# Performance work log

Measured on AMD Instinct MI355X. Metric: run time of the kernel, lower is better.

The kernel has to match this reference:

```python
import jax, jax.numpy as jnp
import numpy as np

DIM = 384
NH = 6
HD = DIM // NH  # 64
WS = (6, 12)    # window_size (dilated_size=[1,1] so total_window_size == window_size)
SS = (3, 6)     # shift_size
N = WS[0] * WS[1]  # 72 tokens per window


def _make_mask(H, W):
    # Faithful replication of SD_attn.create_mask (static, so computed in numpy).
    wh, ww = WS
    sh, sw = SS
    img = np.zeros((H, W), np.float32)
    cnt = 0
    for hs in (slice(0, -wh), slice(-wh, -sh), slice(-sh, None)):
        for wsl in (slice(0, -ww), slice(-ww, 0), slice(0, None)):
            img[hs, wsl] = cnt
            cnt += 1
    # window partition -> (nW, N)
    m = img.reshape(H // wh, wh, W // ww, ww).transpose(0, 2, 1, 3).reshape(-1, wh * ww)
    d = m[:, None, :] - m[:, :, None]  # (nW, N, N), [i,j] = m[j]-m[i]
    return np.where(d != 0, -np.inf, 0.0).astype(np.float32)


def _rope2d(x):
    # 2D axial rotary embedding over the (wh, ww) window grid.
    # x: (M, wh, ww, hd); first half of pair-channels rotated by h-position, second half by w-position.
    wh, ww, hd = x.shape[1], x.shape[2], x.shape[3]
    half = hd // 2
    inv = 1.0 / (10000.0 ** (np.arange(0, half, 2, dtype=np.float32) / half))  # (half//2,)
    ah = np.arange(wh, dtype=np.float32)[:, None] * inv  # (wh, half//2)
    aw = np.arange(ww, dtype=np.float32)[:, None] * inv  # (ww, half//2)
    ang = np.concatenate([
        np.broadcast_to(ah[:, None, :], (wh, ww, half // 2)),
        np.broadcast_to(aw[None, :, :], (wh, ww, half // 2)),
    ], -1)  # (wh, ww, half)
    cos = jnp.asarray(np.cos(ang), dtype=x.dtype)
    sin = jnp.asarray(np.sin(ang), dtype=x.dtype)
    x1, x2 = x[..., 0::2], x[..., 1::2]
    return jnp.stack([x1 * cos - x2 * sin, x1 * sin + x2 * cos], -1).reshape(x.shape)


def setup_inputs() -> dict:
    key = jax.random.key(0)
    ks = jax.random.split(key, 5)
    x = jax.random.normal(ks[0], (2, 192, 384, DIM), jnp.float32)
    w_qkv = 0.02 * jax.random.normal(ks[1], (3 * DIM, DIM), jnp.float32)
    b_qkv = 0.02 * jax.random.normal(ks[2], (3 * DIM,), jnp.float32)
    w_proj = 0.02 * jax.random.normal(ks[3], (DIM, DIM), jnp.float32)
    b_proj = 0.02 * jax.random.normal(ks[4], (DIM,), jnp.float32)
    return {"x": x, "w_qkv": w_qkv, "b_qkv": b_qkv, "w_proj": w_proj, "b_proj": b_proj}


def reference(x, w_qkv, b_qkv, w_proj, b_proj):
    B, H, W, C = x.shape
    wh, ww = WS
    sh, sw = SS
    nH, nWc = H // wh, W // ww
    nwin = nH * nWc
    B_ = B * nwin
    scale = HD ** -0.5

    # cyclic shift + window partition (dilated_size=[1,1] => plain swin windows)
    xs = jnp.roll(x, (-sh, -sw), axis=(1, 2))
    xw = xs.reshape(B, nH, wh, nWc, ww, C).transpose(0, 1, 3, 2, 4, 5).reshape(B_, N, C)

    qkv = (xw @ w_qkv.T + b_qkv).reshape(B_, N, 3, NH, HD).transpose(2, 0, 3, 1, 4)
    q, k, v = qkv[0], qkv[1], qkv[2]  # (B_, NH, N, HD)

    q = _rope2d(q.reshape(-1, wh, ww, HD)).reshape(B_, NH, N, HD)
    k = _rope2d(k.reshape(-1, wh, ww, HD)).reshape(B_, NH, N, HD)

    attn = jnp.einsum('bhnd,bhmd->bhnm', q * scale, k)  # (B_, NH, N, N)
    mask = jnp.asarray(_make_mask(H, W))                 # (nwin, N, N)
    attn = (attn.reshape(B, nwin, NH, N, N) + mask[None, :, None]).reshape(B_, NH, N, N)
    attn = jax.nn.softmax(attn, axis=-1)
    save_attn = attn.mean(axis=1)  # mean over heads -> (B_, N, N)

    out = jnp.einsum('bhnm,bhmd->bhnd', attn, v).transpose(0, 2, 1, 3).reshape(B_, N, C)
    out = out.reshape(B, nH, nWc, wh, ww, C).transpose(0, 1, 3, 2, 4, 5).reshape(B, H, W, C)
    out = jnp.roll(out, (sh, sw), axis=(1, 2))
    out = out @ w_proj.T + b_proj
    return out, save_attn
```

## Files before the change

kernel.cpp:

```cpp
#include <hip/hip_runtime.h>

typedef __attribute__((ext_vector_type(8))) __bf16 bf16x8;
typedef __attribute__((ext_vector_type(4))) float f32x4;
typedef unsigned short u16;
typedef unsigned int u32;

__device__ __forceinline__ u16 f2bf(float x){
  u32 u = __float_as_uint(x);
  return (u16)((u + 0x7fffu + ((u >> 16) & 1u)) >> 16);
}
__device__ __forceinline__ u32 pkbf(float lo, float hi){
  u32 r; asm("v_cvt_pk_bf16_f32 %0, %1, %2" : "=v"(r) : "v"(lo), "v"(hi)); return r;
}

union FragU { uint4 u4; bf16x8 bf; };

__device__ __forceinline__ bf16x8 lds_frag(const unsigned char* smem, int off, int row, int strideB, int kElem){
  int byte = (row * strideB + kElem * 2) ^ ((row & 7) << 4);
  FragU f; f.u4 = *reinterpret_cast<const uint4*>(smem + off + byte);
  return f.bf;
}

typedef __attribute__((address_space(3))) unsigned char lds_u8;
typedef __attribute__((address_space(1))) const unsigned char g_u8;
__device__ __forceinline__ void glds16(const void* g, void* l){
  __builtin_amdgcn_global_load_lds((g_u8*)g, (lds_u8*)l, 16, 0, 0);
}

__global__ void prep_weights(const float* __restrict__ wq, const float* __restrict__ wp,
                             u16* __restrict__ wqb, u16* __restrict__ wpb){
  int i = blockIdx.x * 256 + threadIdx.x;
  wqb[i] = f2bf(wq[i]);
  if (i < 147456) wpb[i] = f2bf(wp[i]);
}

#define QA_OFF 0
#define QB_OFF 16384
#define QTC    65536
#define QTS    66688
__launch_bounds__(512, 2)
__global__ void qkv_gemm(const float* __restrict__ x, const u16* __restrict__ wqb,
                         const float* __restrict__ bq, float* __restrict__ out,
                         u16* __restrict__ vws)
{
  __shared__ __align__(16) unsigned char smem[67840];
  const int tid  = threadIdx.x;
  const int wave = tid >> 6;
  const int lane = tid & 63;
  const int l15  = lane & 15;
  const int lhi  = lane >> 4;
  const int wr   = wave >> 2;
  const int wc   = wave & 3;
  const int bx   = blockIdx.x;
  const int sec  = blockIdx.y;
  const size_t row0 = (size_t)bx * 128;
  const int a    = bx / 3;
  const int bcol = bx - 3 * a;
  const int bIm  = a / 192;
  const int hh   = a % 192;
  const int rh   = (hh >= 3) ? hh - 3 : hh + 189;
  const int wi   = rh / 6;
  const int r6   = rh - wi * 6;
  const int bwin = bIm * 1024 + wi * 32;

  float* tabc = reinterpret_cast<float*>(smem + QTC);
  float* tabs = reinterpret_cast<float*>(smem + QTS);
  if (tid < 288){
    int pos = tid >> 4, m = tid & 15;
    float pv = (pos < 6) ? (float)pos : (float)(pos - 6);
    float ang = pv * __expf(-(float)m * 0.5756462732485114f);
    tabc[tid] = cosf(ang);
    tabs[tid] = sinf(ang);
  }

  f32x4 acc[4][6];
  #pragma unroll
  for (int mt = 0; mt < 4; ++mt)
    #pragma unroll
    for (int nt = 0; nt < 6; ++nt) acc[mt][nt] = 0.0f;

  for (int kk = 0; kk < 6; ++kk){
    {
      int row = tid >> 2;
      int c0  = (tid & 3) << 4;
      const float* src = x + (row0 + row) * 384 + kk * 64 + c0;
      float4 a0 = *reinterpret_cast<const float4*>(src);
      float4 a1 = *reinterpret_cast<const float4*>(src + 4);
      float4 a2 = *reinterpret_cast<const float4*>(src + 8);
      float4 a3 = *reinterpret_cast<const float4*>(src + 12);
      uint4 q0, q1;
      q0.x = pkbf(a0.x, a0.y); q0.y = pkbf(a0.z, a0.w);
      q0.z = pkbf(a1.x, a1.y); q0.w = pkbf(a1.z, a1.w);
      q1.x = pkbf(a2.x, a2.y); q1.y = pkbf(a2.z, a2.w);
      q1.z = pkbf(a3.x, a3.y); q1.w = pkbf(a3.z, a3.w);
      int b0 = (row * 128 + c0 * 2)      ^ ((row & 7) << 4);
      int b1 = (row * 128 + c0 * 2 + 16) ^ ((row & 7) << 4);
      *reinterpret_cast<uint4*>(smem + QA_OFF + b0) = q0;
      *reinterpret_cast<uint4*>(smem + QA_OFF + b1) = q1;
    }
    #pragma unroll
    for (int it = 0; it < 6; ++it){
      int c = it * 512 + tid;
      int n = c >> 3, p = c & 7;
      int s = p ^ (n & 7);
      glds16(wqb + (size_t)(sec * 384 + n) * 384 + kk * 64 + s * 8,
             smem + QB_OFF + c * 16);
    }
    __syncthreads();
    #pragma unroll
    for (int ks = 0; ks < 2; ++ks){
      const int kEl = ks * 32 + lhi * 8;
      bf16x8 af[4], bf[6];
      #pragma unroll
      for (int mt = 0; mt < 4; ++mt)
        af[mt] = lds_frag(smem, QA_OFF, wr * 64 + mt * 16 + l15, 128, kEl);
      #pragma unroll
      for (int nt = 0; nt < 6; ++nt)
        bf[nt] = lds_frag(smem, QB_OFF, wc * 96 + nt * 16 + l15, 128, kEl);
      #pragma unroll
      for (int mt = 0; mt < 4; ++mt)
        #pragma unroll
        for (int nt = 0; nt < 6; ++nt)
          acc[mt][nt] = __builtin_amdgcn_mfma_f32_16x16x32_bf16(af[mt], bf[nt], acc[mt][nt], 0, 0, 0);
    }
    __syncthreads();
  }

  if (sec < 2){
    u16* o16 = (u16*)out;
    #pragma unroll
    for (int nt = 0; nt < 6; ++nt){
      const int ch = wc * 96 + nt * 16 + l15;
      const float bias = bq[sec * 384 + ch];
      const int chh = ch & 63;
      const int p   = chh >> 1;
      const int m   = p & 15;
      const bool isR = (p < 16);
      const bool ev  = ((ch & 1) == 0);
      #pragma unroll
      for (int mt = 0; mt < 4; ++mt){
        #pragma unroll
        for (int r = 0; r < 4; ++r){
          const int i = wr * 64 + mt * 16 + lhi * 4 + r;
          float v = acc[mt][nt][r] + bias;
          float o = __shfl_xor(v, 1);
          int pos = isR ? r6 : (6 + (bcol * 128 + i + 6) % 12);
          float cc = tabc[pos * 16 + m], ssn = tabs[pos * 16 + m];
          float nv = ev ? (v * cc - o * ssn) : (o * ssn + v * cc);
          if (sec == 0) nv *= 0.125f;
          o16[(row0 + i) * 768 + sec * 384 + ch] = f2bf(nv);
        }
      }
    }
  } else {
    #pragma unroll
    for (int mt = 0; mt < 4; ++mt){
      const int ww2 = bcol * 128 + wr * 64 + mt * 16 + lhi * 4;
      const int rw  = (ww2 >= 6) ? ww2 - 6 : ww2 + 378;
      const int wj  = rw / 12;
      const int c0  = rw - wj * 12;
      const int tokb = r6 * 12;
      #pragma unroll
      for (int nt = 0; nt < 6; ++nt){
        const int ch  = wc * 96 + nt * 16 + l15;
        const int h   = ch >> 6;
        const int chh = ch & 63;
        const float bv = bq[768 + ch];
        u32 lo = pkbf(acc[mt][nt][0] + bv, acc[mt][nt][1] + bv);
        u32 hi = pkbf(acc[mt][nt][2] + bv, acc[mt][nt][3] + bv);
        u16* basep = vws + ((size_t)(bwin + wj) * 6 + h) * 5120 + chh * 80;
        if (c0 != 10){
          *reinterpret_cast<u32*>(basep + tokb + c0)     = lo;
          *reinterpret_cast<u32*>(basep + tokb + c0 + 2) = hi;
        } else {
          *reinterpret_cast<u32*>(basep + tokb + 10) = lo;
          const int wj1 = (wj == 31) ? 0 : wj + 1;
          *reinterpret_cast<u32*>(vws + ((size_t)(bwin + wj1) * 6 + h) * 5120 + chh * 80 + tokb) = hi;
        }
      }
    }
  }
}

#define QH4 0
#define KH4 10240
#define VT4 20480
#define SMEM4 30720
__launch_bounds__(320, 5)
__global__ void win_attn4(const u16* __restrict__ vws,
                          float* __restrict__ out)
{
  __shared__ __align__(16) unsigned char smem[SMEM4];
  const int tid  = threadIdx.x;
  const int wave = tid >> 6;
  const int lane = tid & 63;
  const int l15  = lane & 15;
  const int lhi  = lane >> 4;

  const int bid  = blockIdx.x;
  const int wgid = (bid & 7) * 256 + (bid >> 3);
  const int bIdx = wgid >> 10;
  const int win  = wgid & 1023;
  const int wi   = win >> 5;
  const int wj   = win & 31;
  const bool maskWin = (wi == 31);

  auto rowof = [&](int t)->size_t {
    int r = t / 12, c = t - r * 12;
    int hh = wi * 6 + r + 3;  if (hh >= 192) hh -= 192;
    int ww = wj * 12 + c + 6; if (ww >= 384) ww -= 384;
    return ((size_t)bIdx * 192 + hh) * 384 + ww;
  };
  const int qtok = wave * 16 + l15;
  const bool tv = (qtok < 72);
  const size_t qrow = rowof(tv ? qtok : 71);

  const u16* o16c = (const u16*)out;
  u16* ao16 = (u16*)out;
  const u16* vsl = vws + (size_t)win * 30720 + (size_t)bIdx * 31457280;

  float sv[5][4];
  #pragma unroll
  for (int a2 = 0; a2 < 5; ++a2)
    #pragma unroll
    for (int b2 = 0; b2 < 4; ++b2) sv[a2][b2] = 0.0f;

  for (int h = 0; h < 6; ++h){
    #pragma unroll
    for (int it = 0; it < 2; ++it){
      int c = it * 320 + tid;
      int t = c >> 3, p = c & 7;
      size_t row = rowof(t < 72 ? t : 71);
      int s = (p ^ (t & 7)) << 3;
      glds16(o16c + row * 768 + h * 64 + s,       smem + QH4 + c * 16);
      glds16(o16c + row * 768 + 384 + h * 64 + s, smem + KH4 + c * 16);
      glds16(vsl + (size_t)h * 5120 + c * 8,      smem + VT4 + c * 16);
    }
    __syncthreads();

    f32x4 pf[5];
    #pragma unroll
    for (int nt = 0; nt < 5; ++nt) pf[nt] = 0.0f;
    #pragma unroll
    for (int ks = 0; ks < 2; ++ks){
      const int kEl = ks * 32 + lhi * 8;
      bf16x8 qf = lds_frag(smem, QH4, qtok, 128, kEl);
      #pragma unroll
      for (int nt = 0; nt < 5; ++nt){
        bf16x8 kf = lds_frag(smem, KH4, nt * 16 + l15, 128, kEl);
        pf[nt] = __builtin_amdgcn_mfma_f32_16x16x32_bf16(kf, qf, pf[nt], 0, 0, 0);
      }
    }

    float mx = -1e30f;
    #pragma unroll
    for (int nt = 0; nt < 5; ++nt)
      #pragma unroll
      for (int r = 0; r < 4; ++r){
        const int kk2 = nt * 16 + lhi * 4 + r;
        bool valid = (kk2 < 72) && (!maskWin || ((kk2 < 36) == (qtok < 36)));
        float val = valid ? pf[nt][r] : -1e30f;
        pf[nt][r] = val;
        mx = fmaxf(mx, val);
      }
    mx = fmaxf(mx, __shfl_xor(mx, 16));
    mx = fmaxf(mx, __shfl_xor(mx, 32));
    float sm = 0.0f;
    #pragma unroll
    for (int nt = 0; nt < 5; ++nt)
      #pragma unroll
      for (int r = 0; r < 4; ++r){
        float e = __expf(pf[nt][r] - mx);
        pf[nt][r] = e; sm += e;
      }
    sm += __shfl_xor(sm, 16);
    sm += __shfl_xor(sm, 32);
    const float inv = 1.0f / sm;
    u32 pp[5][2];
    #pragma unroll
    for (int nt = 0; nt < 5; ++nt){
      float p0 = pf[nt][0] * inv, p1 = pf[nt][1] * inv;
      float p2 = pf[nt][2] * inv, p3 = pf[nt][3] * inv;
      sv[nt][0] += p0; sv[nt][1] += p1; sv[nt][2] += p2; sv[nt][3] += p3;
      pp[nt][0] = pkbf(p0, p1);
      pp[nt][1] = pkbf(p2, p3);
    }

    f32x4 oacc[4];
    #pragma unroll
    for (int nt = 0; nt < 4; ++nt) oacc[nt] = 0.0f;
    #pragma unroll
    for (int ks = 0; ks < 3; ++ks){
      FragU pb;
      u32 w[4];
      #pragma unroll
      for (int w_ = 0; w_ < 4; ++w_){
        int srcLane = l15 + 16 * ((lane >> 4 & 1) * 2 + (w_ >> 1));
        u32 c0 = __shfl(pp[ks * 2][w_ & 1], srcLane);
        u32 c1 = (ks * 2 + 1 < 5) ? __shfl(pp[ks * 2 + 1][w_ & 1], srcLane) : 0u;
        w[w_] = (lhi & 2) ? c1 : c0;
      }
      pb.u4.x = w[0]; pb.u4.y = w[1]; pb.u4.z = w[2]; pb.u4.w = w[3];
      const int kEl = ks * 32 + lhi * 8;
      #pragma unroll
      for (int nt = 0; nt < 4; ++nt){
        FragU vf;
        vf.u4 = *reinterpret_cast<const uint4*>(smem + VT4 + (nt * 16 + l15) * 160 + kEl * 2);
        oacc[nt] = __builtin_amdgcn_mfma_f32_16x16x32_bf16(vf.bf, pb.bf, oacc[nt], 0, 0, 0);
      }
    }
    if (tv){
      u16* ao = ao16 + qrow * 768 + h * 64;
      #pragma unroll
      for (int nt = 0; nt < 4; ++nt){
        uint2 pk;
        pk.x = pkbf(oacc[nt][0], oacc[nt][1]);
        pk.y = pkbf(oacc[nt][2], oacc[nt][3]);
        *reinterpret_cast<uint2*>(ao + nt * 16 + lhi * 4) = pk;
      }
    }
    __syncthreads();
  }

  if (tv){
    float* so = out + 56623104ull + (size_t)wgid * 5184 + (size_t)qtok * 72;
    const float c6 = 1.0f / 6.0f;
    #pragma unroll
    for (int nt = 0; nt < 4; ++nt){
      float4 v4; v4.x = sv[nt][0]*c6; v4.y = sv[nt][1]*c6; v4.z = sv[nt][2]*c6; v4.w = sv[nt][3]*c6;
      *reinterpret_cast<float4*>(so + nt * 16 + lhi * 4) = v4;
    }
    if (lhi < 2){
      float4 v4; v4.x = sv[4][0]*c6; v4.y = sv[4][1]*c6; v4.z = sv[4][2]*c6; v4.w = sv[4][3]*c6;
      *reinterpret_cast<float4*>(so + 64 + lhi * 4) = v4;
    }
  }
}

#define VT3 0
#define P3  16384
__launch_bounds__(320, 4)
__global__ void win_attn_fb(const float* __restrict__ x,
                            const u16* __restrict__ wqb,
                            const float* __restrict__ bq,
                            float* __restrict__ out)
{
  __shared__ __align__(16) unsigned char smem[36864];
  const int tid  = threadIdx.x;
  const int wave = tid >> 6;
  const int lane = tid & 63;
  const int l15  = lane & 15;
  const int lhi  = lane >> 4;

  const int wgid = blockIdx.x;
  const int bIdx = wgid >> 10;
  const int win  = wgid & 1023;
  const int wi   = win >> 5;
  const int wj   = win & 31;
  const bool maskWin = (wi == 31);

  auto rowof = [&](int t)->int {
    int r = t / 12, c = t - r * 12;
    int hh = wi * 6 + r + 3;  if (hh >= 192) hh -= 192;
    int ww = wj * 12 + c + 6; if (ww >= 384) ww -= 384;
    return (bIdx * 192 + hh) * 384 + ww;
  };
  const int qtok = wave * 16 + l15;
  const int qrow = rowof(qtok < 72 ? qtok : 71);
  int krow[5];
  #pragma unroll
  for (int nt = 0; nt < 5; ++nt) krow[nt] = rowof(nt * 16 + l15 < 72 ? nt * 16 + l15 : 71);
  const bool tv = (qtok < 72);

  bf16x8 xfrag[12];
  {
    const float* xp = x + (size_t)qrow * 384;
    #pragma unroll
    for (int ks = 0; ks < 12; ++ks){
      uint4 q; q.x = 0; q.y = 0; q.z = 0; q.w = 0;
      if (tv){
        float4 f0 = *reinterpret_cast<const float4*>(xp + ks * 32 + lhi * 8);
        float4 f1 = *reinterpret_cast<const float4*>(xp + ks * 32 + lhi * 8 + 4);
        q.x = pkbf(f0.x, f0.y); q.y = pkbf(f0.z, f0.w);
        q.z = pkbf(f1.x, f1.y); q.w = pkbf(f1.z, f1.w);
      }
      FragU f; f.u4 = q; xfrag[ks] = f.bf;
    }
  }

  const u16* o16 = (const u16*)out;
  u16* ao16 = (u16*)out;
  const u16* wv = wqb + 768 * 384;

  float sv[5][4];
  #pragma unroll
  for (int a2 = 0; a2 < 5; ++a2)
    #pragma unroll
    for (int b2 = 0; b2 < 4; ++b2) sv[a2][b2] = 0.0f;

  for (int h = 0; h < 6; ++h){
    {
      f32x4 vacc[4];
      #pragma unroll
      for (int nt = 0; nt < 4; ++nt) vacc[nt] = 0.0f;
      #pragma unroll
      for (int ks = 0; ks < 12; ++ks){
        const int kEl = ks * 32 + lhi * 8;
        #pragma unroll
        for (int nt = 0; nt < 4; ++nt){
          FragU f;
          f.u4 = *reinterpret_cast<const uint4*>(wv + (size_t)(h * 64 + nt * 16 + l15) * 384 + kEl);
          vacc[nt] = __builtin_amdgcn_mfma_f32_16x16x32_bf16(xfrag[ks], f.bf, vacc[nt], 0, 0, 0);
        }
      }
      #pragma unroll
      for (int nt = 0; nt < 4; ++nt){
        const int chl = nt * 16 + l15;
        const float bv = bq[768 + h * 64 + chl];
        const int t0 = wave * 16 + lhi * 4;
        uint2 pk;
        pk.x = pkbf(vacc[nt][0] + bv, vacc[nt][1] + bv);
        pk.y = pkbf(vacc[nt][2] + bv, vacc[nt][3] + bv);
        int byte = (chl * 256 + t0 * 2) ^ ((chl & 7) << 4);
        *reinterpret_cast<uint2*>(smem + VT3 + byte) = pk;
      }
    }

    f32x4 pf[5];
    #pragma unroll
    for (int nt = 0; nt < 5; ++nt) pf[nt] = 0.0f;
    #pragma unroll
    for (int ks = 0; ks < 2; ++ks){
      const int kEl = ks * 32 + lhi * 8;
      FragU qf;
      qf.u4 = *reinterpret_cast<const uint4*>(o16 + (size_t)qrow * 768 + h * 64 + kEl);
      #pragma unroll
      for (int nt = 0; nt < 5; ++nt){
        FragU kf;
        kf.u4 = *reinterpret_cast<const uint4*>(o16 + (size_t)krow[nt] * 768 + 384 + h * 64 + kEl);
        pf[nt] = __builtin_amdgcn_mfma_f32_16x16x32_bf16(kf.bf, qf.bf, pf[nt], 0, 0, 0);
      }
    }

    float mx = -1e30f;
    #pragma unroll
    for (int nt = 0; nt < 5; ++nt)
      #pragma unroll
      for (int r = 0; r < 4; ++r){
        const int kk2 = nt * 16 + lhi * 4 + r;
        bool valid = (kk2 < 72) && (!maskWin || ((kk2 < 36) == (qtok < 36)));
        float val = valid ? pf[nt][r] : -1e30f;
        pf[nt][r] = val;
        mx = fmaxf(mx, val);
      }
    mx = fmaxf(mx, __shfl_xor(mx, 16));
    mx = fmaxf(mx, __shfl_xor(mx, 32));
    float sm = 0.0f;
    #pragma unroll
    for (int nt = 0; nt < 5; ++nt)
      #pragma unroll
      for (int r = 0; r < 4; ++r){
        float e = __expf(pf[nt][r] - mx);
        pf[nt][r] = e; sm += e;
      }
    sm += __shfl_xor(sm, 16);
    sm += __shfl_xor(sm, 32);
    const float inv = 1.0f / sm;
    #pragma unroll
    for (int nt = 0; nt < 5; ++nt)
      #pragma unroll
      for (int r = 0; r < 4; ++r){
        float pv2 = pf[nt][r] * inv;
        pf[nt][r] = pv2;
        sv[nt][r] += pv2;
      }

    #pragma unroll
    for (int nt = 0; nt < 5; ++nt){
      const int k0 = nt * 16 + lhi * 4;
      uint2 pk;
      pk.x = pkbf(pf[nt][0], pf[nt][1]);
      pk.y = pkbf(pf[nt][2], pf[nt][3]);
      int byte = (qtok * 256 + k0 * 2) ^ ((qtok & 7) << 4);
      *reinterpret_cast<uint2*>(smem + P3 + byte) = pk;
    }
    {
      int byte = (qtok * 256 + (80 + lhi * 4) * 2) ^ ((qtok & 7) << 4);
      uint2 z; z.x = 0; z.y = 0;
      *reinterpret_cast<uint2*>(smem + P3 + byte) = z;
    }
    __syncthreads();

    f32x4 oacc[4];
    #pragma unroll
    for (int nt = 0; nt < 4; ++nt) oacc[nt] = 0.0f;
    #pragma unroll
    for (int ks = 0; ks < 3; ++ks){
      const int kEl = ks * 32 + lhi * 8;
      bf16x8 pfr = lds_frag(smem, P3, qtok, 256, kEl);
      #pragma unroll
      for (int nt = 0; nt < 4; ++nt){
        bf16x8 vf = lds_frag(smem, VT3, nt * 16 + l15, 256, kEl);
        oacc[nt] = __builtin_amdgcn_mfma_f32_16x16x32_bf16(vf, pfr, oacc[nt], 0, 0, 0);
      }
    }
    if (tv){
      u16* ao = ao16 + (size_t)qrow * 768 + h * 64;
      #pragma unroll
      for (int nt = 0; nt < 4; ++nt){
        uint2 pk;
        pk.x = pkbf(oacc[nt][0], oacc[nt][1]);
        pk.y = pkbf(oacc[nt][2], oacc[nt][3]);
        *reinterpret_cast<uint2*>(ao + nt * 16 + lhi * 4) = pk;
      }
    }
    __syncthreads();
  }

  if (tv){
    float* so = out + 56623104ull + (size_t)wgid * 5184 + (size_t)qtok * 72;
    const float c6 = 1.0f / 6.0f;
    #pragma unroll
    for (int nt = 0; nt < 4; ++nt){
      float4 v4; v4.x = sv[nt][0]*c6; v4.y = sv[nt][1]*c6; v4.z = sv[nt][2]*c6; v4.w = sv[nt][3]*c6;
      *reinterpret_cast<float4*>(so + nt * 16 + lhi * 4) = v4;
    }
    if (lhi < 2){
      float4 v4; v4.x = sv[4][0]*c6; v4.y = sv[4][1]*c6; v4.z = sv[4][2]*c6; v4.w = sv[4][3]*c6;
      *reinterpret_cast<float4*>(so + 64 + lhi * 4) = v4;
    }
  }
}

#define A2_OFF 0
#define B2_OFF 16384
#define SMEM2  65536
__launch_bounds__(512, 2)
__global__ void proj_gemm(const u16* __restrict__ wpb, const float* __restrict__ bp,
                          float* __restrict__ out)
{
  __shared__ __align__(16) unsigned char smem[SMEM2];
  unsigned char* base = smem;

  const int tid  = threadIdx.x;
  const int wave = tid >> 6;
  const int lane = tid & 63;
  const int l15  = lane & 15;
  const int lhi  = lane >> 4;
  const int wr   = wave >> 2;
  const int wc   = wave & 3;
  const size_t row0 = (size_t)blockIdx.x * 128;
  const u16* aog = (const u16*)out;

  f32x4 acc[4][6];
  #pragma unroll
  for (int mt = 0; mt < 4; ++mt)
    #pragma unroll
    for (int nt = 0; nt < 6; ++nt) acc[mt][nt] = 0.0f;

  for (int kk = 0; kk < 6; ++kk){
    #pragma unroll
    for (int it = 0; it < 2; ++it){
      int c = it * 512 + wave * 64 + lane;
      int rrow = c >> 3, p = c & 7;
      int s = p ^ (rrow & 7);
      glds16(aog + (row0 + rrow) * 768 + kk * 64 + s * 8,
             base + A2_OFF + (it * 512 + wave * 64) * 16);
    }
    #pragma unroll
    for (int it = 0; it < 6; ++it){
      int c = it * 512 + wave * 64 + lane;
      int n = c >> 3, p = c & 7;
      int s = p ^ (n & 7);
      glds16(wpb + (size_t)n * 384 + kk * 64 + s * 8,
             base + B2_OFF + (it * 512 + wave * 64) * 16);
    }
    __syncthreads();
    #pragma unroll
    for (int ks = 0; ks < 2; ++ks){
      const int kEl = ks * 32 + lhi * 8;
      bf16x8 af[4], bf[6];
      #pragma unroll
      for (int mt = 0; mt < 4; ++mt)
        af[mt] = lds_frag(base, A2_OFF, wr * 64 + mt * 16 + l15, 128, kEl);
      #pragma unroll
      for (int nt = 0; nt < 6; ++nt)
        bf[nt] = lds_frag(base, B2_OFF, wc * 96 + nt * 16 + l15, 128, kEl);
      #pragma unroll
      for (int mt = 0; mt < 4; ++mt)
        #pragma unroll
        for (int nt = 0; nt < 6; ++nt)
          acc[mt][nt] = __builtin_amdgcn_mfma_f32_16x16x32_bf16(af[mt], bf[nt], acc[mt][nt], 0, 0, 0);
    }
    __syncthreads();
  }

  float bpv[6];
  #pragma unroll
  for (int nt = 0; nt < 6; ++nt) bpv[nt] = bp[wc * 96 + nt * 16 + l15];
  #pragma unroll
  for (int mt = 0; mt < 4; ++mt)
    #pragma unroll
    for (int nt = 0; nt < 6; ++nt){
      const int ch = wc * 96 + nt * 16 + l15;
      #pragma unroll
      for (int r = 0; r < 4; ++r){
        size_t grow = row0 + wr * 64 + mt * 16 + lhi * 4 + r;
        out[grow * 384 + ch] = acc[mt][nt][r] + bpv[nt];
      }
    }
}

extern "C" void kernel_launch(void* const* d_in, const int* in_sizes, int n_in,
                              void* d_out, int out_size, void* d_ws, size_t ws_size,
                              hipStream_t stream)
{
  const float* x  = (const float*)d_in[0];
  const float* wq = (const float*)d_in[1];
  const float* bq = (const float*)d_in[2];
  const float* wp = (const float*)d_in[3];
  const float* bp = (const float*)d_in[4];
  float* out = (float*)d_out;

  u16* wqb = (u16*)d_ws;
  u16* wpb = (u16*)((char*)d_ws + 442368 * 2);
  u16* vws = (u16*)((char*)d_ws + 1179648);

  const bool big = ws_size >= 127008768ull;

  prep_weights<<<1728, 256, 0, stream>>>(wq, wp, wqb, wpb);
  if (big){
    qkv_gemm<<<dim3(1152, 3), 512, 0, stream>>>(x, wqb, bq, out, vws);
    win_attn4<<<2048, 320, 0, stream>>>(vws, out);
  } else {
    qkv_gemm<<<dim3(1152, 2), 512, 0, stream>>>(x, wqb, bq, out, vws);
    win_attn_fb<<<2048, 320, 0, stream>>>(x, wqb, bq, out);
  }
  proj_gemm<<<1152, 512, 0, stream>>>(wpb, bp, out);
}
```

Measured before the change: 692.0 us.

## Pre-convert x to bf16 and load QKV GEMM A-tiles via direct LDS loads

Adds a prep kernel that converts x to bf16 once into workspace. When the workspace is large enough, the QKV GEMM then streams bf16 A tiles straight into LDS with global_load_lds instead of loading fp32 and converting per tile. Each of the three y-sections previously re-read and re-converted the fp32 input, so this is meant to halve those reads and drop the conversion work. It also raises wave priority around the MFMA blocks in window attention. The cost is an extra full pass over x plus a new bf16 copy in memory, and the path only runs if the harness workspace is large enough.

```diff
diff --git a/kernel.cpp b/kernel.cpp
--- a/kernel.cpp
+++ b/kernel.cpp
@@ -34,14 +34,26 @@
   if (i < 147456) wpb[i] = f2bf(wp[i]);
 }
 
+__global__ void prep_x(const float* __restrict__ x, u16* __restrict__ xb){
+  size_t i = ((size_t)blockIdx.x * 256 + threadIdx.x) * 8;
+  float4 f0 = *reinterpret_cast<const float4*>(x + i);
+  float4 f1 = *reinterpret_cast<const float4*>(x + i + 4);
+  uint4 q;
+  q.x = pkbf(f0.x, f0.y); q.y = pkbf(f0.z, f0.w);
+  q.z = pkbf(f1.x, f1.y); q.w = pkbf(f1.z, f1.w);
+  *reinterpret_cast<uint4*>(xb + i) = q;
+}
+
 #define QA_OFF 0
 #define QB_OFF 16384
 #define QTC    65536
 #define QTS    66688
+template<int XB>
 __launch_bounds__(512, 2)
-__global__ void qkv_gemm(const float* __restrict__ x, const u16* __restrict__ wqb,
-                         const float* __restrict__ bq, float* __restrict__ out,
-                         u16* __restrict__ vws)
+__global__ void qkv_gemm_t(const float* __restrict__ x, const u16* __restrict__ xb,
+                           const u16* __restrict__ wqb,
+                           const float* __restrict__ bq, float* __restrict__ out,
+                           u16* __restrict__ vws)
 {
   __shared__ __align__(16) unsigned char smem[67840];
   const int tid  = threadIdx.x;
@@ -80,7 +92,16 @@
     for (int nt = 0; nt < 6; ++nt) acc[mt][nt] = 0.0f;
 
   for (int kk = 0; kk < 6; ++kk){
-    {
+    if constexpr (XB){
+      #pragma unroll
+      for (int it = 0; it < 2; ++it){
+        int c = it * 512 + tid;
+        int rrow = c >> 3, p = c & 7;
+        int s = p ^ (rrow & 7);
+        glds16(xb + (row0 + rrow) * 384 + kk * 64 + s * 8,
+               smem + QA_OFF + c * 16);
+      }
+    } else {
       int row = tid >> 2;
       int c0  = (tid & 3) << 4;
       const float* src = x + (row0 + row) * 384 + kk * 64 + c0;
@@ -241,6 +262,7 @@
     f32x4 pf[5];
     #pragma unroll
     for (int nt = 0; nt < 5; ++nt) pf[nt] = 0.0f;
+    __builtin_amdgcn_s_setprio(1);
     #pragma unroll
     for (int ks = 0; ks < 2; ++ks){
       const int kEl = ks * 32 + lhi * 8;
@@ -251,6 +273,7 @@
         pf[nt] = __builtin_amdgcn_mfma_f32_16x16x32_bf16(kf, qf, pf[nt], 0, 0, 0);
       }
     }
+    __builtin_amdgcn_s_setprio(0);
 
     float mx = -1e30f;
     #pragma unroll
@@ -302,12 +325,14 @@
       }
       pb.u4.x = w[0]; pb.u4.y = w[1]; pb.u4.z = w[2]; pb.u4.w = w[3];
       const int kEl = ks * 32 + lhi * 8;
+      __builtin_amdgcn_s_setprio(1);
       #pragma unroll
       for (int nt = 0; nt < 4; ++nt){
         FragU vf;
         vf.u4 = *reinterpret_cast<const uint4*>(smem + VT4 + (nt * 16 + l15) * 160 + kEl * 2);
         oacc[nt] = __builtin_amdgcn_mfma_f32_16x16x32_bf16(vf.bf, pb.bf, oacc[nt], 0, 0, 0);
       }
+      __builtin_amdgcn_s_setprio(0);
     }
     if (tv){
       u16* ao = ao16 + qrow * 768 + h * 64;
@@ -625,15 +650,21 @@
   u16* wqb = (u16*)d_ws;
   u16* wpb = (u16*)((char*)d_ws + 442368 * 2);
   u16* vws = (u16*)((char*)d_ws + 1179648);
-
-  const bool big = ws_size >= 127008768ull;
+  u16* xb  = (u16*)((char*)d_ws + 127008768);
+
+  const bool big  = ws_size >= 127008768ull;
+  const bool big2 = ws_size >= 240254976ull;
 
   prep_weights<<<1728, 256, 0, stream>>>(wq, wp, wqb, wpb);
-  if (big){
-    qkv_gemm<<<dim3(1152, 3), 512, 0, stream>>>(x, wqb, bq, out, vws);
+  if (big2){
+    prep_x<<<27648, 256, 0, stream>>>(x, xb);
+    qkv_gemm_t<1><<<dim3(1152, 3), 512, 0, stream>>>(x, xb, wqb, bq, out, vws);
+    win_attn4<<<2048, 320, 0, stream>>>(vws, out);
+  } else if (big){
+    qkv_gemm_t<0><<<dim3(1152, 3), 512, 0, stream>>>(x, nullptr, wqb, bq, out, vws);
     win_attn4<<<2048, 320, 0, stream>>>(vws, out);
   } else {
-    qkv_gemm<<<dim3(1152, 2), 512, 0, stream>>>(x, wqb, bq, out, vws);
+    qkv_gemm_t<0><<<dim3(1152, 2), 512, 0, stream>>>(x, nullptr, wqb, bq, out, vws);
     win_attn_fb<<<2048, 320, 0, stream>>>(x, wqb, bq, out);
   }
   proj_gemm<<<1152, 512, 0, stream>>>(wpb, bp, out);
```

After: 710.9 us. 2.7% more time.
